# Performance work log

Hardware: AMD Instinct MI355X
Metric: run time of the kernel (lower is better)

The kernel has to match this reference:

```python
import jax, jax.numpy as jnp
import numpy as np

D_MODEL = 1024
NUM_HEADS = 16
D_K = D_MODEL // NUM_HEADS


def setup_inputs() -> dict:
    key = jax.random.key(0)
    ks = jax.random.split(key, 11)
    B, S, D = 2, 2048, D_MODEL
    s = 1.0 / np.sqrt(D)
    return {
        "Q": jax.random.normal(ks[0], (B, S, D), jnp.float32),
        "K": jax.random.normal(ks[1], (B, S, D), jnp.float32),
        "V": jax.random.normal(ks[2], (B, S, D), jnp.float32),
        "Wq": jax.random.normal(ks[3], (D, D), jnp.float32) * s,
        "bq": jax.random.normal(ks[4], (D,), jnp.float32) * s,
        "Wk": jax.random.normal(ks[5], (D, D), jnp.float32) * s,
        "bk": jax.random.normal(ks[6], (D,), jnp.float32) * s,
        "Wv": jax.random.normal(ks[7], (D, D), jnp.float32) * s,
        "bv": jax.random.normal(ks[8], (D,), jnp.float32) * s,
        "Wo": jax.random.normal(ks[9], (D, D), jnp.float32) * s,
        "bo": jax.random.normal(ks[10], (D,), jnp.float32) * s,
    }


def reference(Q, K, V, Wq, bq, Wk, bk, Wv, bv, Wo, bo):
    B, S, D = Q.shape
    H, dk = NUM_HEADS, D_K
    scale = 1.0 / np.sqrt(dk)

    def split_heads(x):  # (B,S,D) -> (B,H,S,dk)
        return x.reshape(B, S, H, dk).transpose(0, 2, 1, 3)

    q = split_heads(Q @ Wq.T + bq)
    k = split_heads(K @ Wk.T + bk)
    v = split_heads(V @ Wv.T + bv)

    scores = jnp.einsum("bhqd,bhkd->bhqk", q, k) * scale
    attn_weights = jax.nn.softmax(scores, axis=-1)
    attn_out = jnp.einsum("bhqk,bhkd->bhqd", attn_weights, v)
    attn_out = attn_out.transpose(0, 2, 1, 3).reshape(B, S, D)
    output = attn_out @ Wo.T + bo
    return (output, attn_weights)
```

## Files before the change

kernel.cpp:

```cpp
#include <hip/hip_runtime.h>

typedef unsigned short u16;
typedef unsigned int u32;
typedef unsigned long long u64;
typedef float f32x4 __attribute__((ext_vector_type(4)));
typedef __bf16 bf16x8 __attribute__((ext_vector_type(8)));
typedef unsigned short u16x8 __attribute__((ext_vector_type(8)));
typedef unsigned short u16x4 __attribute__((ext_vector_type(4)));

#define DEV static __device__ __forceinline__

DEV u16 f2bf(float f) {
  __bf16 h = (__bf16)f;
  union { __bf16 h; u16 u; } x; x.h = h;
  return x.u;
}

DEV float fexp2(float x) { return __builtin_amdgcn_exp2f(x); }

DEV f32x4 mfma16(bf16x8 a, bf16x8 b, f32x4 c) {
  return __builtin_amdgcn_mfma_f32_16x16x32_bf16(a, b, c, 0, 0, 0);
}

DEV void gl_lds16(const u16* g, void* l) {
  __builtin_amdgcn_global_load_lds(
      (const __attribute__((address_space(1))) void*)(const void*)g,
      (__attribute__((address_space(3))) void*)l, 16, 0, 0);
}

struct PrepArgs { const float* s[16]; u16* d[16]; };

__global__ __launch_bounds__(256) void k_prep(PrepArgs p) {
  int bid = blockIdx.x, seg = bid >> 9;
  const float* __restrict__ s = p.s[seg];
  u16* __restrict__ d = p.d[seg];
  int i = ((bid & 511) << 11) + threadIdx.x * 8;
  f32x4 v0 = *(const f32x4*)(s + i);
  f32x4 v1 = *(const f32x4*)(s + i + 4);
  u16x8 o;
#pragma unroll
  for (int j = 0; j < 4; ++j) { o[j] = f2bf(v0[j]); o[4 + j] = f2bf(v1[j]); }
  *(u16x8*)(d + i) = o;
}

struct GArgs {
  const u16* A[3]; const u16* B[3]; const float* bias[3];
  void* C[3]; float post;
};

template<int BM, int MODE>
__global__ __launch_bounds__(256) void k_gemm(GArgs a) {
  constexpr int WTM = BM / 32;
  constexpr int NXY = (4096 / BM) * 8;
  constexpr int NB = (MODE == 1) ? 3 * NXY : NXY;
  __shared__ u16 a_lds[BM * 64];
  __shared__ u16 b_lds[128 * 64];

  const int t = threadIdx.x, lane = t & 63, wid = t >> 6;
  const int wm = wid & 1, wn = wid >> 1;
  const int fid = blockIdx.x;
  const int v = (fid & 7) * (NB >> 3) + (fid >> 3);
  int z, rr;
  if (MODE == 1) { z = v / NXY; rr = v % NXY; } else { z = 0; rr = v; }
  const int xb = rr >> 3, yb = rr & 7;

  const u16* __restrict__ Ab = a.A[z];
  const u16* __restrict__ Bb = a.B[z];

  f32x4 acc[WTM][4] = {};
  const int fr = lane & 15, g = (lane >> 4) & 3;
  const int c8s = (lane & 7) ^ ((lane >> 3) & 7);
  const int r8 = lane >> 3;

  for (int kt = 0; kt < 16; ++kt) {
#pragma unroll
    for (int j = 0; j < BM / 32; ++j) {
      int row = wid * (BM / 4) + j * 8 + r8;
      gl_lds16(Ab + (long)(xb * BM + row) * 1024 + kt * 64 + c8s * 8,
               (char*)a_lds + wid * (BM * 32) + j * 1024);
    }
#pragma unroll
    for (int j = 0; j < 4; ++j) {
      int row = wid * 32 + j * 8 + r8;
      gl_lds16(Bb + (long)(yb * 128 + row) * 1024 + kt * 64 + c8s * 8,
               (char*)b_lds + wid * 4096 + j * 1024);
    }
    __syncthreads();
#pragma unroll
    for (int kk = 0; kk < 2; ++kk) {
      const int csw = ((kk * 4 + g) ^ (fr & 7)) << 4;
      bf16x8 af[WTM], bq[4];
#pragma unroll
      for (int mi = 0; mi < WTM; ++mi)
        af[mi] = *(const bf16x8*)((const char*)a_lds +
                 (wm * (BM / 2) + mi * 16 + fr) * 128 + csw);
#pragma unroll
      for (int ni = 0; ni < 4; ++ni)
        bq[ni] = *(const bf16x8*)((const char*)b_lds +
                 (wn * 64 + ni * 16 + fr) * 128 + csw);
#pragma unroll
      for (int mi = 0; mi < WTM; ++mi)
#pragma unroll
        for (int ni = 0; ni < 4; ++ni)
          acc[mi][ni] = mfma16(af[mi], bq[ni], acc[mi][ni]);
    }
    __syncthreads();
  }

  const int r4 = ((lane >> 4) & 3) * 4, cc = lane & 15;
  const float* __restrict__ bias = a.bias[z];
  const float post = (MODE == 1 && z == 0) ? a.post : 1.0f;

#pragma unroll
  for (int mi = 0; mi < WTM; ++mi)
#pragma unroll
  for (int ni = 0; ni < 4; ++ni) {
    const int col = yb * 128 + wn * 64 + ni * 16 + cc;
    const float bv = bias[col];
    const int row0 = xb * BM + wm * (BM / 2) + mi * 16 + r4;
    if (MODE == 0) {
      float* O = (float*)a.C[0];
#pragma unroll
      for (int rg = 0; rg < 4; ++rg)
        O[(long)(row0 + rg) * 1024 + col] = acc[mi][ni][rg] + bv;
    } else if (z < 2) {
      u16* O = (u16*)a.C[z];
#pragma unroll
      for (int rg = 0; rg < 4; ++rg) {
        int row = row0 + rg;
        int b = row >> 11, s = row & 2047, h = col >> 6, d = col & 63;
        O[(((long)(b * 16 + h) * 2048 + s) << 6) + d] =
            f2bf((acc[mi][ni][rg] + bv) * post);
      }
    } else {
      u16* O = (u16*)a.C[2];
      int b = row0 >> 11, s = row0 & 2047, h = col >> 6, d = col & 63;
      u16x4 o;
#pragma unroll
      for (int rg = 0; rg < 4; ++rg) o[rg] = f2bf(acc[mi][ni][rg] + bv);
      *(u16x4*)&O[((long)(b * 16 + h) * 64 + d) * 2048 + s] = o;
    }
  }
}

__global__ __launch_bounds__(256, 2) void k_fused_attn(
    const u16* __restrict__ QP, const u16* __restrict__ KP,
    const u16* __restrict__ VPT, float* __restrict__ attn,
    u16* __restrict__ AO)
{
  __shared__ u16 k_lds[2][128 * 64];
  __shared__ u16 vt_lds[2][64 * 128];
  __shared__ u16 p_lds[4 * 16 * 128];

  const int t = threadIdx.x, lane = t & 63, w = t >> 6;
  const int fr = lane & 15, g = lane >> 4;
  const int zz = blockIdx.z;
  const int b = zz >> 4, h = zz & 15;
  const int q0 = blockIdx.x * 128;
  const long headQK = (long)zz * (2048 * 64);
  const long headVT = (long)zz * (64 * 2048);
  const int c8s = (lane & 7) ^ ((lane >> 3) & 7);
  const int r8 = lane >> 3;

  auto stageK = [&](int buf, int kt) {
#pragma unroll
    for (int j = 0; j < 4; ++j) {
      int row = w * 32 + j * 8 + r8;
      gl_lds16(KP + headQK + (long)(kt * 128 + row) * 64 + c8s * 8,
               (char*)k_lds[buf] + w * 4096 + j * 1024);
    }
  };
  auto stageV = [&](int buf, int kt) {
#pragma unroll
    for (int j = 0; j < 4; ++j) {
      int row = w * 16 + j * 4 + (lane >> 4);
      int c16s = (lane & 15) ^ (row & 7);
      gl_lds16(VPT + headVT + (long)row * 2048 + kt * 128 + c16s * 8,
               (char*)vt_lds[buf] + w * 4096 + j * 1024);
    }
  };

  bf16x8 aq[2][2];
#pragma unroll
  for (int mi = 0; mi < 2; ++mi)
#pragma unroll
    for (int kk = 0; kk < 2; ++kk)
      aq[mi][kk] = *(const bf16x8*)&QP[headQK +
          (long)(q0 + w * 32 + mi * 16 + fr) * 64 + kk * 32 + g * 8];

  float l[2] = {0.f, 0.f};

  stageK(0, 0);
  __syncthreads();
  for (int kt = 0; kt < 16; ++kt) {
    const int cur = kt & 1;
    if (kt < 15) stageK(cur ^ 1, kt + 1);
#pragma unroll
    for (int mi = 0; mi < 2; ++mi) {
      float s = 0.f;
#pragma unroll
      for (int ni = 0; ni < 8; ++ni) {
        f32x4 c = (f32x4){};
#pragma unroll
        for (int kk = 0; kk < 2; ++kk) {
          bf16x8 bk = *(const bf16x8*)((const char*)k_lds[cur] +
                      (ni * 16 + fr) * 128 + (((kk * 4 + g) ^ (fr & 7)) << 4));
          c = mfma16(bk, aq[mi][kk], c);
        }
#pragma unroll
        for (int rg = 0; rg < 4; ++rg) s += fexp2(c[rg]);
      }
      l[mi] += s;
    }
    __syncthreads();
  }

  stageK(0, 0);
  stageV(0, 0);
  float invl[2];
#pragma unroll
  for (int mi = 0; mi < 2; ++mi) {
    float lo = l[mi];
    lo += __shfl_xor(lo, 16);
    lo += __shfl_xor(lo, 32);
    invl[mi] = 1.0f / lo;
  }
  f32x4 acc[2][4] = {};
  char* pw = (char*)&p_lds[w * 2048];
  const int qrow_base = q0 + w * 32 + fr;
  __syncthreads();

  for (int kt = 0; kt < 16; ++kt) {
    const int cur = kt & 1;
    if (kt < 15) { stageK(cur ^ 1, kt + 1); stageV(cur ^ 1, kt + 1); }

#pragma unroll
    for (int mi = 0; mi < 2; ++mi) {
      const long arow = ((long)zz * 2048 + qrow_base + mi * 16) * 2048 + kt * 128;
#pragma unroll
      for (int ni = 0; ni < 8; ++ni) {
        f32x4 c = (f32x4){};
#pragma unroll
        for (int kk = 0; kk < 2; ++kk) {
          bf16x8 bk = *(const bf16x8*)((const char*)k_lds[cur] +
                      (ni * 16 + fr) * 128 + (((kk * 4 + g) ^ (fr & 7)) << 4));
          c = mfma16(bk, aq[mi][kk], c);
        }
        f32x4 p;
#pragma unroll
        for (int rg = 0; rg < 4; ++rg)
          p[rg] = fexp2(c[rg]) * invl[mi];
        __builtin_nontemporal_store(p, (f32x4*)&attn[arow + ni * 16 + g * 4]);
        union { u16x4 us; u64 ull; } pk;
#pragma unroll
        for (int rg = 0; rg < 4; ++rg) pk.us[rg] = f2bf(p[rg]);
        int byte = (fr << 8) + ((ni * 16 + g * 4) << 1);
        byte ^= (fr & 7) << 4;
        *(u64*)(pw + byte) = pk.ull;
      }
#pragma unroll
      for (int kk = 0; kk < 4; ++kk) {
        int byte = (fr << 8) + ((kk * 32 + g * 8) << 1);
        byte ^= (fr & 7) << 4;
        bf16x8 pa = *(const bf16x8*)(pw + byte);
#pragma unroll
        for (int di = 0; di < 4; ++di) {
          bf16x8 bv = *(const bf16x8*)((const char*)vt_lds[cur] +
                      (di * 16 + fr) * 256 + (((kk * 4 + g) ^ (fr & 7)) << 4));
          acc[mi][di] = mfma16(pa, bv, acc[mi][di]);
        }
      }
    }
    __syncthreads();
  }

#pragma unroll
  for (int mi = 0; mi < 2; ++mi)
#pragma unroll
  for (int di = 0; di < 4; ++di)
#pragma unroll
  for (int rg = 0; rg < 4; ++rg) {
    int row = q0 + w * 32 + mi * 16 + g * 4 + rg;
    AO[((long)b * 2048 + row) * 1024 + h * 64 + di * 16 + fr] =
        f2bf(acc[mi][di][rg]);
  }
}

extern "C" void kernel_launch(void* const* d_in, const int* in_sizes, int n_in,
                              void* d_out, int out_size, void* d_ws, size_t ws_size,
                              hipStream_t stream) {
  const float* Q  = (const float*)d_in[0];
  const float* Kx = (const float*)d_in[1];
  const float* V  = (const float*)d_in[2];
  const float* Wq = (const float*)d_in[3];
  const float* bq = (const float*)d_in[4];
  const float* Wk = (const float*)d_in[5];
  const float* bk = (const float*)d_in[6];
  const float* Wv = (const float*)d_in[7];
  const float* bv = (const float*)d_in[8];
  const float* Wo = (const float*)d_in[9];
  const float* bo = (const float*)d_in[10];

  float* out  = (float*)d_out;
  float* attn = out + (long)4 * 1024 * 1024;

  char* ws = (char*)d_ws;
  const long MB = 1 << 20;
  u16* Qb  = (u16*)(ws + 0 * MB);
  u16* Kb  = (u16*)(ws + 8 * MB);
  u16* Wqb = (u16*)(ws + 16 * MB);
  u16* Wkb = (u16*)(ws + 18 * MB);
  u16* Wvb = (u16*)(ws + 20 * MB);
  u16* Wob = (u16*)(ws + 22 * MB);
  u16* QP  = (u16*)(ws + 24 * MB);
  u16* KP  = (u16*)(ws + 32 * MB);
  u16* VPT = (u16*)(ws + 40 * MB);
  u16* AO  = (u16*)(ws + 0 * MB);
  u16* Vb  = (u16*)attn;

  const int M1 = 1 << 20;
  PrepArgs pa;
  for (int j = 0; j < 4; ++j) { pa.s[j] = Q + (long)j * M1;      pa.d[j] = Qb + (long)j * M1; }
  for (int j = 0; j < 4; ++j) { pa.s[4 + j] = Kx + (long)j * M1; pa.d[4 + j] = Kb + (long)j * M1; }
  for (int j = 0; j < 4; ++j) { pa.s[8 + j] = V + (long)j * M1;  pa.d[8 + j] = Vb + (long)j * M1; }
  pa.s[12] = Wq; pa.d[12] = Wqb;
  pa.s[13] = Wk; pa.d[13] = Wkb;
  pa.s[14] = Wv; pa.d[14] = Wvb;
  pa.s[15] = Wo; pa.d[15] = Wob;
  k_prep<<<8192, 256, 0, stream>>>(pa);

  GArgs gq;
  gq.A[0] = Qb; gq.A[1] = Kb; gq.A[2] = Vb;
  gq.B[0] = Wqb; gq.B[1] = Wkb; gq.B[2] = Wvb;
  gq.bias[0] = bq; gq.bias[1] = bk; gq.bias[2] = bv;
  gq.C[0] = QP; gq.C[1] = KP; gq.C[2] = VPT;
  gq.post = 0.125f * 1.4426950408889634f;
  k_gemm<128, 1><<<768, 256, 0, stream>>>(gq);

  k_fused_attn<<<dim3(16, 1, 32), 256, 0, stream>>>(QP, KP, VPT, attn, AO);

  GArgs go;
  go.A[0] = AO; go.A[1] = AO; go.A[2] = AO;
  go.B[0] = Wob; go.B[1] = Wob; go.B[2] = Wob;
  go.bias[0] = bo; go.bias[1] = bo; go.bias[2] = bo;
  go.C[0] = out; go.C[1] = out; go.C[2] = out;
  go.post = 1.0f;
  k_gemm<64, 0><<<512, 256, 0, stream>>>(go);
}
```

Before: 286.3 us.

## Halve attention query tile, drop LDS double buffering, raise occupancy

The fused attention kernel now gives each block 64 query rows (16 per wave) instead of 128, doubling the grid to 1024 blocks. K/V staging becomes single-buffered with barriers around each load, and launch bounds rise to 3 blocks per CU. The aim is more resident waves and better load balance to hide latency. In exchange, each K/V tile is reloaded twice as often per query, the explicit prefetch overlap is gone, and the attn stores lose the nontemporal hint.

```diff
diff --git a/kernel.cpp b/kernel.cpp
--- a/kernel.cpp
+++ b/kernel.cpp
@@ -143,146 +143,128 @@
   }
 }
 
-__global__ __launch_bounds__(256, 2) void k_fused_attn(
+__global__ __launch_bounds__(256, 3) void k_fused_attn(
     const u16* __restrict__ QP, const u16* __restrict__ KP,
     const u16* __restrict__ VPT, float* __restrict__ attn,
     u16* __restrict__ AO)
 {
-  __shared__ u16 k_lds[2][128 * 64];
-  __shared__ u16 vt_lds[2][64 * 128];
+  __shared__ u16 k_lds[128 * 64];
+  __shared__ u16 vt_lds[64 * 128];
   __shared__ u16 p_lds[4 * 16 * 128];
 
   const int t = threadIdx.x, lane = t & 63, w = t >> 6;
   const int fr = lane & 15, g = lane >> 4;
   const int zz = blockIdx.z;
   const int b = zz >> 4, h = zz & 15;
-  const int q0 = blockIdx.x * 128;
+  const int q0 = blockIdx.x * 64;
   const long headQK = (long)zz * (2048 * 64);
   const long headVT = (long)zz * (64 * 2048);
   const int c8s = (lane & 7) ^ ((lane >> 3) & 7);
   const int r8 = lane >> 3;
 
-  auto stageK = [&](int buf, int kt) {
+  auto stageK = [&](int kt) {
 #pragma unroll
     for (int j = 0; j < 4; ++j) {
       int row = w * 32 + j * 8 + r8;
       gl_lds16(KP + headQK + (long)(kt * 128 + row) * 64 + c8s * 8,
-               (char*)k_lds[buf] + w * 4096 + j * 1024);
+               (char*)k_lds + w * 4096 + j * 1024);
     }
   };
-  auto stageV = [&](int buf, int kt) {
+  auto stageV = [&](int kt) {
 #pragma unroll
     for (int j = 0; j < 4; ++j) {
       int row = w * 16 + j * 4 + (lane >> 4);
       int c16s = (lane & 15) ^ (row & 7);
       gl_lds16(VPT + headVT + (long)row * 2048 + kt * 128 + c16s * 8,
-               (char*)vt_lds[buf] + w * 4096 + j * 1024);
+               (char*)vt_lds + w * 4096 + j * 1024);
     }
   };
 
-  bf16x8 aq[2][2];
-#pragma unroll
-  for (int mi = 0; mi < 2; ++mi)
-#pragma unroll
-    for (int kk = 0; kk < 2; ++kk)
-      aq[mi][kk] = *(const bf16x8*)&QP[headQK +
-          (long)(q0 + w * 32 + mi * 16 + fr) * 64 + kk * 32 + g * 8];
-
-  float l[2] = {0.f, 0.f};
-
-  stageK(0, 0);
-  __syncthreads();
+  bf16x8 aq[2];
+#pragma unroll
+  for (int kk = 0; kk < 2; ++kk)
+    aq[kk] = *(const bf16x8*)&QP[headQK +
+        (long)(q0 + w * 16 + fr) * 64 + kk * 32 + g * 8];
+
+  float l = 0.f;
+
   for (int kt = 0; kt < 16; ++kt) {
-    const int cur = kt & 1;
-    if (kt < 15) stageK(cur ^ 1, kt + 1);
-#pragma unroll
-    for (int mi = 0; mi < 2; ++mi) {
-      float s = 0.f;
-#pragma unroll
-      for (int ni = 0; ni < 8; ++ni) {
-        f32x4 c = (f32x4){};
-#pragma unroll
-        for (int kk = 0; kk < 2; ++kk) {
-          bf16x8 bk = *(const bf16x8*)((const char*)k_lds[cur] +
-                      (ni * 16 + fr) * 128 + (((kk * 4 + g) ^ (fr & 7)) << 4));
-          c = mfma16(bk, aq[mi][kk], c);
-        }
-#pragma unroll
-        for (int rg = 0; rg < 4; ++rg) s += fexp2(c[rg]);
+    __syncthreads();
+    stageK(kt);
+    __syncthreads();
+    float s = 0.f;
+#pragma unroll
+    for (int ni = 0; ni < 8; ++ni) {
+      f32x4 c = (f32x4){};
+#pragma unroll
+      for (int kk = 0; kk < 2; ++kk) {
+        bf16x8 bk = *(const bf16x8*)((const char*)k_lds +
+                    (ni * 16 + fr) * 128 + (((kk * 4 + g) ^ (fr & 7)) << 4));
+        c = mfma16(bk, aq[kk], c);
       }
-      l[mi] += s;
-    }
-    __syncthreads();
-  }
-
-  stageK(0, 0);
-  stageV(0, 0);
-  float invl[2];
-#pragma unroll
-  for (int mi = 0; mi < 2; ++mi) {
-    float lo = l[mi];
-    lo += __shfl_xor(lo, 16);
-    lo += __shfl_xor(lo, 32);
-    invl[mi] = 1.0f / lo;
-  }
-  f32x4 acc[2][4] = {};
+#pragma unroll
+      for (int rg = 0; rg < 4; ++rg) s += fexp2(c[rg]);
+    }
+    l += s;
+  }
+
+  l += __shfl_xor(l, 16);
+  l += __shfl_xor(l, 32);
+  const float invl = 1.0f / l;
+
+  f32x4 acc[4] = {};
   char* pw = (char*)&p_lds[w * 2048];
-  const int qrow_base = q0 + w * 32 + fr;
-  __syncthreads();
+  const int qrow_base = q0 + w * 16 + fr;
 
   for (int kt = 0; kt < 16; ++kt) {
-    const int cur = kt & 1;
-    if (kt < 15) { stageK(cur ^ 1, kt + 1); stageV(cur ^ 1, kt + 1); }
-
-#pragma unroll
-    for (int mi = 0; mi < 2; ++mi) {
-      const long arow = ((long)zz * 2048 + qrow_base + mi * 16) * 2048 + kt * 128;
-#pragma unroll
-      for (int ni = 0; ni < 8; ++ni) {
-        f32x4 c = (f32x4){};
-#pragma unroll
-        for (int kk = 0; kk < 2; ++kk) {
-          bf16x8 bk = *(const bf16x8*)((const char*)k_lds[cur] +
-                      (ni * 16 + fr) * 128 + (((kk * 4 + g) ^ (fr & 7)) << 4));
-          c = mfma16(bk, aq[mi][kk], c);
-        }
-        f32x4 p;
-#pragma unroll
-        for (int rg = 0; rg < 4; ++rg)
-          p[rg] = fexp2(c[rg]) * invl[mi];
-        __builtin_nontemporal_store(p, (f32x4*)&attn[arow + ni * 16 + g * 4]);
-        union { u16x4 us; u64 ull; } pk;
-#pragma unroll
-        for (int rg = 0; rg < 4; ++rg) pk.us[rg] = f2bf(p[rg]);
-        int byte = (fr << 8) + ((ni * 16 + g * 4) << 1);
-        byte ^= (fr & 7) << 4;
-        *(u64*)(pw + byte) = pk.ull;
+    __syncthreads();
+    stageK(kt);
+    stageV(kt);
+    __syncthreads();
+
+    const long arow = ((long)zz * 2048 + qrow_base) * 2048 + kt * 128;
+#pragma unroll
+    for (int ni = 0; ni < 8; ++ni) {
+      f32x4 c = (f32x4){};
+#pragma unroll
+      for (int kk = 0; kk < 2; ++kk) {
+        bf16x8 bk = *(const bf16x8*)((const char*)k_lds +
+                    (ni * 16 + fr) * 128 + (((kk * 4 + g) ^ (fr & 7)) << 4));
+        c = mfma16(bk, aq[kk], c);
       }
-#pragma unroll
-      for (int kk = 0; kk < 4; ++kk) {
-        int byte = (fr << 8) + ((kk * 32 + g * 8) << 1);
-        byte ^= (fr & 7) << 4;
-        bf16x8 pa = *(const bf16x8*)(pw + byte);
-#pragma unroll
-        for (int di = 0; di < 4; ++di) {
-          bf16x8 bv = *(const bf16x8*)((const char*)vt_lds[cur] +
-                      (di * 16 + fr) * 256 + (((kk * 4 + g) ^ (fr & 7)) << 4));
-          acc[mi][di] = mfma16(pa, bv, acc[mi][di]);
-        }
+      f32x4 p;
+#pragma unroll
+      for (int rg = 0; rg < 4; ++rg)
+        p[rg] = fexp2(c[rg]) * invl;
+      *(f32x4*)&attn[arow + ni * 16 + g * 4] = p;
+      union { u16x4 us; u64 ull; } pk;
+#pragma unroll
+      for (int rg = 0; rg < 4; ++rg) pk.us[rg] = f2bf(p[rg]);
+      int byte = (fr << 8) + ((ni * 16 + g * 4) << 1);
+      byte ^= (fr & 7) << 4;
+      *(u64*)(pw + byte) = pk.ull;
+    }
+#pragma unroll
+    for (int kk = 0; kk < 4; ++kk) {
+      int byte = (fr << 8) + ((kk * 32 + g * 8) << 1);
+      byte ^= (fr & 7) << 4;
+      bf16x8 pa = *(const bf16x8*)(pw + byte);
+#pragma unroll
+      for (int di = 0; di < 4; ++di) {
+        bf16x8 bv = *(const bf16x8*)((const char*)vt_lds +
+                    (di * 16 + fr) * 256 + (((kk * 4 + g) ^ (fr & 7)) << 4));
+        acc[di] = mfma16(pa, bv, acc[di]);
       }
     }
-    __syncthreads();
-  }
-
-#pragma unroll
-  for (int mi = 0; mi < 2; ++mi)
+  }
+
 #pragma unroll
   for (int di = 0; di < 4; ++di)
 #pragma unroll
   for (int rg = 0; rg < 4; ++rg) {
-    int row = q0 + w * 32 + mi * 16 + g * 4 + rg;
+    int row = q0 + w * 16 + g * 4 + rg;
     AO[((long)b * 2048 + row) * 1024 + h * 64 + di * 16 + fr] =
-        f2bf(acc[mi][di][rg]);
+        f2bf(acc[di][rg]);
   }
 }
 
@@ -337,7 +319,7 @@
   gq.post = 0.125f * 1.4426950408889634f;
   k_gemm<128, 1><<<768, 256, 0, stream>>>(gq);
 
-  k_fused_attn<<<dim3(16, 1, 32), 256, 0, stream>>>(QP, KP, VPT, attn, AO);
+  k_fused_attn<<<dim3(32, 1, 32), 256, 0, stream>>>(QP, KP, VPT, attn, AO);
 
   GArgs go;
   go.A[0] = AO; go.A[1] = AO; go.A[2] = AO;
```

New measurement: 283.5 us. About the same (-1.0%).

## Load K and V fragments directly from global memory instead of LDS staging

Applied to the files above, without the earlier changes.

Removes the double-buffered LDS staging of K and V tiles and their block-wide barriers. Each wave now reads its MFMA operand fragments straight from global memory (relying on L1/L2 for reuse across waves) and reuses each K fragment across both query sub-tiles. The P buffer is enlarged per wave so both sub-tiles are kept before the PV product. The attention-weight store changes from a nontemporal store to a normal store. The cost is redundant global/cache traffic, since four waves each fetch the same K/V data, and exposed load latency without software prefetch.

```diff
diff --git a/kernel.cpp b/kernel.cpp
--- a/kernel.cpp
+++ b/kernel.cpp
@@ -148,9 +148,7 @@
     const u16* __restrict__ VPT, float* __restrict__ attn,
     u16* __restrict__ AO)
 {
-  __shared__ u16 k_lds[2][128 * 64];
-  __shared__ u16 vt_lds[2][64 * 128];
-  __shared__ u16 p_lds[4 * 16 * 128];
+  __shared__ u16 p_lds[4 * 2 * 16 * 128];
 
   const int t = threadIdx.x, lane = t & 63, w = t >> 6;
   const int fr = lane & 15, g = lane >> 4;
@@ -159,26 +157,9 @@
   const int q0 = blockIdx.x * 128;
   const long headQK = (long)zz * (2048 * 64);
   const long headVT = (long)zz * (64 * 2048);
-  const int c8s = (lane & 7) ^ ((lane >> 3) & 7);
-  const int r8 = lane >> 3;
-
-  auto stageK = [&](int buf, int kt) {
-#pragma unroll
-    for (int j = 0; j < 4; ++j) {
-      int row = w * 32 + j * 8 + r8;
-      gl_lds16(KP + headQK + (long)(kt * 128 + row) * 64 + c8s * 8,
-               (char*)k_lds[buf] + w * 4096 + j * 1024);
-    }
-  };
-  auto stageV = [&](int buf, int kt) {
-#pragma unroll
-    for (int j = 0; j < 4; ++j) {
-      int row = w * 16 + j * 4 + (lane >> 4);
-      int c16s = (lane & 15) ^ (row & 7);
-      gl_lds16(VPT + headVT + (long)row * 2048 + kt * 128 + c16s * 8,
-               (char*)vt_lds[buf] + w * 4096 + j * 1024);
-    }
-  };
+
+  const u16* __restrict__ Kf = KP + headQK + (long)fr * 64 + g * 8;
+  const u16* __restrict__ Vf = VPT + headVT + (long)fr * 2048 + g * 8;
 
   bf16x8 aq[2][2];
 #pragma unroll
@@ -190,33 +171,22 @@
 
   float l[2] = {0.f, 0.f};
 
-  stageK(0, 0);
-  __syncthreads();
   for (int kt = 0; kt < 16; ++kt) {
-    const int cur = kt & 1;
-    if (kt < 15) stageK(cur ^ 1, kt + 1);
-#pragma unroll
-    for (int mi = 0; mi < 2; ++mi) {
-      float s = 0.f;
-#pragma unroll
-      for (int ni = 0; ni < 8; ++ni) {
-        f32x4 c = (f32x4){};
-#pragma unroll
-        for (int kk = 0; kk < 2; ++kk) {
-          bf16x8 bk = *(const bf16x8*)((const char*)k_lds[cur] +
-                      (ni * 16 + fr) * 128 + (((kk * 4 + g) ^ (fr & 7)) << 4));
-          c = mfma16(bk, aq[mi][kk], c);
-        }
-#pragma unroll
-        for (int rg = 0; rg < 4; ++rg) s += fexp2(c[rg]);
+    const u16* kp = Kf + kt * 8192;
+#pragma unroll
+    for (int ni = 0; ni < 8; ++ni) {
+      bf16x8 bk0 = *(const bf16x8*)(kp + ni * 1024);
+      bf16x8 bk1 = *(const bf16x8*)(kp + ni * 1024 + 32);
+#pragma unroll
+      for (int mi = 0; mi < 2; ++mi) {
+        f32x4 c = mfma16(bk0, aq[mi][0], (f32x4){});
+        c = mfma16(bk1, aq[mi][1], c);
+        float s = fexp2(c[0]) + fexp2(c[1]) + fexp2(c[2]) + fexp2(c[3]);
+        l[mi] += s;
       }
-      l[mi] += s;
-    }
-    __syncthreads();
-  }
-
-  stageK(0, 0);
-  stageV(0, 0);
+    }
+  }
+
   float invl[2];
 #pragma unroll
   for (int mi = 0; mi < 2; ++mi) {
@@ -225,53 +195,51 @@
     lo += __shfl_xor(lo, 32);
     invl[mi] = 1.0f / lo;
   }
+
   f32x4 acc[2][4] = {};
-  char* pw = (char*)&p_lds[w * 2048];
+  char* pw = (char*)&p_lds[w * 8192 / 2];
   const int qrow_base = q0 + w * 32 + fr;
-  __syncthreads();
 
   for (int kt = 0; kt < 16; ++kt) {
-    const int cur = kt & 1;
-    if (kt < 15) { stageK(cur ^ 1, kt + 1); stageV(cur ^ 1, kt + 1); }
-
-#pragma unroll
-    for (int mi = 0; mi < 2; ++mi) {
-      const long arow = ((long)zz * 2048 + qrow_base + mi * 16) * 2048 + kt * 128;
-#pragma unroll
-      for (int ni = 0; ni < 8; ++ni) {
-        f32x4 c = (f32x4){};
-#pragma unroll
-        for (int kk = 0; kk < 2; ++kk) {
-          bf16x8 bk = *(const bf16x8*)((const char*)k_lds[cur] +
-                      (ni * 16 + fr) * 128 + (((kk * 4 + g) ^ (fr & 7)) << 4));
-          c = mfma16(bk, aq[mi][kk], c);
-        }
+    const u16* kp = Kf + kt * 8192;
+#pragma unroll
+    for (int ni = 0; ni < 8; ++ni) {
+      bf16x8 bk0 = *(const bf16x8*)(kp + ni * 1024);
+      bf16x8 bk1 = *(const bf16x8*)(kp + ni * 1024 + 32);
+#pragma unroll
+      for (int mi = 0; mi < 2; ++mi) {
+        f32x4 c = mfma16(bk0, aq[mi][0], (f32x4){});
+        c = mfma16(bk1, aq[mi][1], c);
         f32x4 p;
 #pragma unroll
         for (int rg = 0; rg < 4; ++rg)
           p[rg] = fexp2(c[rg]) * invl[mi];
-        __builtin_nontemporal_store(p, (f32x4*)&attn[arow + ni * 16 + g * 4]);
+        *(f32x4*)&attn[((long)zz * 2048 + qrow_base + mi * 16) * 2048 +
+                       kt * 128 + ni * 16 + g * 4] = p;
         union { u16x4 us; u64 ull; } pk;
 #pragma unroll
         for (int rg = 0; rg < 4; ++rg) pk.us[rg] = f2bf(p[rg]);
-        int byte = (fr << 8) + ((ni * 16 + g * 4) << 1);
+        int byte = (mi << 12) + (fr << 8) + ((ni * 16 + g * 4) << 1);
         byte ^= (fr & 7) << 4;
         *(u64*)(pw + byte) = pk.ull;
       }
-#pragma unroll
-      for (int kk = 0; kk < 4; ++kk) {
-        int byte = (fr << 8) + ((kk * 32 + g * 8) << 1);
+    }
+#pragma unroll
+    for (int kk = 0; kk < 4; ++kk) {
+      bf16x8 bv[4];
+#pragma unroll
+      for (int di = 0; di < 4; ++di)
+        bv[di] = *(const bf16x8*)(Vf + (long)di * 32768 + kt * 128 + kk * 32);
+#pragma unroll
+      for (int mi = 0; mi < 2; ++mi) {
+        int byte = (mi << 12) + (fr << 8) + ((kk * 32 + g * 8) << 1);
         byte ^= (fr & 7) << 4;
         bf16x8 pa = *(const bf16x8*)(pw + byte);
 #pragma unroll
-        for (int di = 0; di < 4; ++di) {
-          bf16x8 bv = *(const bf16x8*)((const char*)vt_lds[cur] +
-                      (di * 16 + fr) * 256 + (((kk * 4 + g) ^ (fr & 7)) << 4));
-          acc[mi][di] = mfma16(pa, bv, acc[mi][di]);
-        }
+        for (int di = 0; di < 4; ++di)
+          acc[mi][di] = mfma16(pa, bv[di], acc[mi][di]);
       }
     }
-    __syncthreads();
   }
 
 #pragma unroll
```

Result: slower. 418.9 us (+46.3%).
